# Kernel tuning notes

Hardware: AMD Instinct MI355X
Metric: run time of the kernel (lower is better)

The kernel has to match this reference:

```python
import jax, jax.numpy as jnp
import numpy as np
import math

B, SQ, SK, H, NH = 8, 512, 512, 768, 12
DH = H // NH

def setup_inputs() -> dict:
    key = jax.random.key(0)
    ks = jax.random.split(key, 8)
    s = 1.0 / math.sqrt(H)
    return {
        "hidden_states": jax.random.normal(ks[0], (B, SQ, H), jnp.float32),
        "context": jax.random.normal(ks[1], (B, SK, H), jnp.float32),
        "attention_mask": jax.random.randint(ks[2], (B, SK), 0, 2, jnp.int32),
        "Wq": jax.random.normal(ks[3], (H, H), jnp.float32) * s,
        "bq": jnp.zeros((H,), jnp.float32),
        "Wk": jax.random.normal(ks[4], (H, H), jnp.float32) * s,
        "bk": jnp.zeros((H,), jnp.float32),
        "Wv": jax.random.normal(ks[5], (H, H), jnp.float32) * s,
        "bv": jnp.zeros((H,), jnp.float32),
        "abs_pos_emb": jax.random.normal(ks[6], (512, DH), jnp.float32),
    }

def _heads(x):
    # [B, S, H] -> [B, NH, S, DH]
    b, s, _ = x.shape
    return x.reshape(b, s, NH, DH).transpose(0, 2, 1, 3)

def reference(hidden_states, context, attention_mask, Wq, bq, Wk, bk, Wv, bv, abs_pos_emb):
    q = _heads(hidden_states @ Wq.T + bq)   # [B,NH,SQ,DH]
    k = _heads(context @ Wk.T + bk)         # [B,NH,SK,DH]
    v = _heads(context @ Wv.T + bv)         # [B,NH,SK,DH]
    scores = jnp.einsum('bhqd,bhkd->bhqk', q, k)
    pos_k = abs_pos_emb[:context.shape[1]]          # [SK, DH]
    pos_q = abs_pos_emb[:hidden_states.shape[1]]    # [SQ, DH]
    pos_scores = jnp.einsum('bhqd,kd->bhqk', q + pos_q[None, None], pos_k)
    scores = (scores + pos_scores) / jnp.sqrt(jnp.float32(DH))
    mask_bias = jnp.where(attention_mask[:, None, None, :] == 0,
                          -jnp.inf, 0.0).astype(scores.dtype)
    scores = scores + mask_bias
    probs = jax.nn.softmax(scores, axis=-1)  # dropout is identity in eval
    out = jnp.einsum('bhqk,bhkd->bhqd', probs, v)
    b, _, sq, _ = out.shape
    return out.transpose(0, 2, 1, 3).reshape(b, sq, NH * DH)
```

## Files before the change

### kernel.cpp

```cpp
#include <hip/hip_runtime.h>
#include <stdint.h>

#define B_   8
#define SQ_  512
#define SK_  512
#define H_   768
#define NH_  12
#define DH_  64
#define BH_  (B_*NH_)
#define M_   (B_*SQ_)
#define NTOT (3*H_)

typedef __attribute__((ext_vector_type(8))) short short8;
typedef __attribute__((ext_vector_type(4))) float floatx4;
typedef __attribute__((ext_vector_type(4))) unsigned int uint4v;
typedef __attribute__((ext_vector_type(4))) unsigned short ushort4v;

#define MFMA16(a, b, c) __builtin_amdgcn_mfma_f32_16x16x32_bf16((a), (b), (c), 0, 0, 0)

__device__ __forceinline__ unsigned short f2b(float f) {
  union { float f; unsigned u; } c; c.f = f;
  unsigned r = (c.u + 0x7fffu + ((c.u >> 16) & 1u)) >> 16;
  return (unsigned short)r;
}
__device__ __forceinline__ float b2f(unsigned short u) {
  union { float f; unsigned u; } c; c.u = ((unsigned)u) << 16;
  return c.f;
}
__device__ __forceinline__ short8 ld8(const unsigned short* p) {
  union { uint4v u; short8 s; } c;
  c.u = *(const uint4v*)p;
  return c.s;
}

#define SEG_X   (M_*H_)
#define SEG_XC  (2*SEG_X)
#define SEG_W1  (H_*H_)
#define SEG_WE  (SEG_XC + 3*SEG_W1)
#define SEG_BE  (SEG_WE + NTOT)
#define SEG_PE  (SEG_BE + SQ_*DH_)

__global__ __launch_bounds__(256) void pack_kernel(
    const float* __restrict__ hid, const float* __restrict__ ctx,
    const float* __restrict__ Wq, const float* __restrict__ Wk, const float* __restrict__ Wv,
    const float* __restrict__ bq, const float* __restrict__ bk, const float* __restrict__ bv,
    const float* __restrict__ pos,
    unsigned short* __restrict__ Xh, unsigned short* __restrict__ Xc,
    unsigned short* __restrict__ Wa, float* __restrict__ Ba,
    unsigned short* __restrict__ Pb)
{
  int i = (blockIdx.x * 256 + threadIdx.x) * 4;
  if (i < SEG_X) {
    floatx4 v = *(const floatx4*)(hid + i);
    ushort4v o = { f2b(v.x), f2b(v.y), f2b(v.z), f2b(v.w) };
    *(ushort4v*)(Xh + i) = o;
  } else if (i < SEG_XC) {
    int j = i - SEG_X;
    floatx4 v = *(const floatx4*)(ctx + j);
    ushort4v o = { f2b(v.x), f2b(v.y), f2b(v.z), f2b(v.w) };
    *(ushort4v*)(Xc + j) = o;
  } else if (i < SEG_WE) {
    int j = i - SEG_XC;
    const float* src; int o;
    if (j < SEG_W1)        { src = Wq; o = j; }
    else if (j < 2*SEG_W1) { src = Wk; o = j - SEG_W1; }
    else                   { src = Wv; o = j - 2*SEG_W1; }
    floatx4 v = *(const floatx4*)(src + o);
    ushort4v ov = { f2b(v.x), f2b(v.y), f2b(v.z), f2b(v.w) };
    *(ushort4v*)(Wa + j) = ov;
  } else if (i < SEG_BE) {
    int j = i - SEG_WE;
    #pragma unroll
    for (int t = 0; t < 4; ++t) {
      int jj = j + t;
      float v = (jj < H_) ? bq[jj] : (jj < 2*H_) ? bk[jj - H_] : bv[jj - 2*H_];
      Ba[jj] = v;
    }
  } else if (i < SEG_PE) {
    int j = i - SEG_BE;
    floatx4 v = *(const floatx4*)(pos + j);
    ushort4v o = { f2b(v.x), f2b(v.y), f2b(v.z), f2b(v.w) };
    *(ushort4v*)(Pb + j) = o;
  }
}

__global__ __launch_bounds__(256) void qkv_gemm(
    const unsigned short* __restrict__ Xh, const unsigned short* __restrict__ Xc,
    const unsigned short* __restrict__ W,  const float* __restrict__ bias,
    const unsigned short* __restrict__ Pb,
    unsigned short* __restrict__ qw, unsigned short* __restrict__ kw,
    unsigned short* __restrict__ vt)
{
  __shared__ unsigned short As[128][72];
  __shared__ unsigned short Bs[128][72];

  int bx = blockIdx.x;
  int bn = bx % 18, bm = bx / 18;
  const unsigned short* X = (bn < 6) ? Xh : Xc;
  bool isV = (bn >= 12);
  int m0 = bm * 128, n0 = bn * 128;

  int tid = threadIdx.x;
  int lane = tid & 63, wave = tid >> 6;
  int wm = (wave & 1) * 64, wn = (wave >> 1) * 64;
  int lc16 = lane & 15, quad = lane >> 4, kk = quad * 8;
  int srow = tid >> 3, sch = (tid & 7) * 8;

  unsigned short (*TA)[72] = isV ? As : Bs;
  unsigned short (*TB)[72] = isV ? Bs : As;
  int oa = isV ? wm : wn;
  int ob = isV ? wn : wm;

  floatx4 acc[4][4];
  #pragma unroll
  for (int i = 0; i < 4; ++i)
    #pragma unroll
    for (int j = 0; j < 4; ++j) acc[i][j] = (floatx4){0.f, 0.f, 0.f, 0.f};

  for (int k0 = 0; k0 < H_; k0 += 64) {
    uint4v a[4], b[4];
    #pragma unroll
    for (int rp = 0; rp < 4; ++rp) {
      a[rp] = *(const uint4v*)&X[(m0 + srow + rp * 32) * H_ + k0 + sch];
      b[rp] = *(const uint4v*)&W[(n0 + srow + rp * 32) * H_ + k0 + sch];
    }
    __syncthreads();
    #pragma unroll
    for (int rp = 0; rp < 4; ++rp) {
      *(uint4v*)&As[srow + rp * 32][sch] = a[rp];
      *(uint4v*)&Bs[srow + rp * 32][sch] = b[rp];
    }
    __syncthreads();

    #pragma unroll
    for (int s = 0; s < 2; ++s) {
      short8 af[4], bf[4];
      #pragma unroll
      for (int i = 0; i < 4; ++i) af[i] = ld8(&TA[oa + i * 16 + lc16][s * 32 + kk]);
      #pragma unroll
      for (int i = 0; i < 4; ++i) bf[i] = ld8(&TB[ob + i * 16 + lc16][s * 32 + kk]);
      #pragma unroll
      for (int mi = 0; mi < 4; ++mi)
        #pragma unroll
        for (int ni = 0; ni < 4; ++ni)
          acc[mi][ni] = MFMA16(af[mi], bf[ni], acc[mi][ni]);
    }
  }

  if (!isV) {
    #pragma unroll
    for (int mi = 0; mi < 4; ++mi) {
      #pragma unroll
      for (int ni = 0; ni < 4; ++ni) {
        int gn0 = n0 + wn + mi * 16 + quad * 4;
        int gs  = m0 + wm + ni * 16 + lc16;
        int bidx = gs >> 9, s0 = gs & 511;
        floatx4 bv4 = *(const floatx4*)&bias[gn0];
        ushort4v o;
        if (gn0 < H_) {
          int h = gn0 >> 6, d0 = gn0 & 63;
          #pragma unroll
          for (int r = 0; r < 4; ++r) o[r] = f2b(acc[mi][ni][r] + bv4[r]);
          *(ushort4v*)(qw + (((bidx * NH_ + h) << 9) + s0) * DH_ + d0) = o;
        } else {
          int g = gn0 - H_;
          int h = g >> 6, d0 = g & 63;
          ushort4v pk = *(const ushort4v*)(Pb + s0 * DH_ + d0);
          #pragma unroll
          for (int r = 0; r < 4; ++r) o[r] = f2b(acc[mi][ni][r] + bv4[r] + b2f(pk[r]));
          *(ushort4v*)(kw + (((bidx * NH_ + h) << 9) + s0) * DH_ + d0) = o;
        }
      }
    }
  } else {
    #pragma unroll
    for (int mi = 0; mi < 4; ++mi) {
      #pragma unroll
      for (int ni = 0; ni < 4; ++ni) {
        int gm0 = m0 + wm + mi * 16 + quad * 4;
        int gn  = n0 + wn + ni * 16 + lc16;
        float bv = bias[gn];
        int bidx = gm0 >> 9, s0 = gm0 & 511;
        int g = gn - 2 * H_;
        int h = g >> 6, d = g & 63;
        ushort4v pk;
        #pragma unroll
        for (int r = 0; r < 4; ++r) pk[r] = f2b(acc[mi][ni][r] + bv);
        *(ushort4v*)(vt + ((bidx * NH_ + h) * DH_ + d) * SK_ + s0) = pk;
      }
    }
  }
}

#define SCALE2 0.18033688011112042f
#define CPAD 136

__global__ __launch_bounds__(256) void attn_kernel(
    const unsigned short* __restrict__ qw, const unsigned short* __restrict__ kw,
    const unsigned short* __restrict__ vt, const unsigned short* __restrict__ posb,
    const int* __restrict__ mask, float* __restrict__ out)
{
  __shared__ unsigned short Sc[64][CPAD];
  __shared__ float mb2[SK_];
  __shared__ float red[64][4];

  int bx = blockIdx.x;
  int bh = bx >> 3, qt = bx & 7;
  int b = bh / NH_, h = bh - b * NH_;
  int tid = threadIdx.x, lane = tid & 63, wave = tid >> 6;
  int lc16 = lane & 15, quad = lane >> 4, kk = quad * 8;

  for (int i = tid; i < SK_; i += 256)
    mb2[i] = mask[(b << 9) + i] ? 0.0f : -100000.0f;

  const unsigned short* qbase = qw + ((bh << 9) + qt * 64) * DH_;
  const unsigned short* pqb   = posb + (qt * 64) * DH_;
  short8 aq[4][2], ap[4][2];
  #pragma unroll
  for (int rt = 0; rt < 4; ++rt) {
    const unsigned short* qr = qbase + (rt * 16 + lc16) * DH_;
    const unsigned short* pr = pqb + (rt * 16 + lc16) * DH_;
    aq[rt][0] = ld8(qr + kk);
    aq[rt][1] = ld8(qr + 32 + kk);
    ap[rt][0] = ld8(pr + kk);
    ap[rt][1] = ld8(pr + 32 + kk);
  }

  const unsigned short* vb0 = vt + (bh * DH_ + wave * 16 + lc16) * SK_;
  float rs[4] = {0.f, 0.f, 0.f, 0.f};
  floatx4 o[4];
  #pragma unroll
  for (int i = 0; i < 4; ++i) o[i] = (floatx4){0.f, 0.f, 0.f, 0.f};

  __syncthreads();

  for (int chunk = 0; chunk < 4; ++chunk) {
    #pragma unroll
    for (int ct = 0; ct < 2; ++ct) {
      int kcol = chunk * 128 + wave * 32 + ct * 16;
      const unsigned short* kb = kw + ((bh << 9) + kcol) * DH_;
      const unsigned short* pb = posb + kcol * DH_;
      short8 b0 = ld8(kb + lc16 * DH_ + kk);
      short8 b1 = ld8(kb + lc16 * DH_ + 32 + kk);
      short8 p0 = ld8(pb + lc16 * DH_ + kk);
      short8 p1 = ld8(pb + lc16 * DH_ + 32 + kk);
      floatx4 mk = *(const floatx4*)&mb2[kcol + quad * 4];
      floatx4 c[4];
      #pragma unroll
      for (int rt = 0; rt < 4; ++rt) {
        c[rt] = (floatx4){0.f, 0.f, 0.f, 0.f};
        c[rt] = MFMA16(b0, aq[rt][0], c[rt]);
        c[rt] = MFMA16(b1, aq[rt][1], c[rt]);
        c[rt] = MFMA16(p0, ap[rt][0], c[rt]);
        c[rt] = MFMA16(p1, ap[rt][1], c[rt]);
      }
      int lcol = wave * 32 + ct * 16 + quad * 4;
      #pragma unroll
      for (int rt = 0; rt < 4; ++rt) {
        ushort4v pv;
        float s = 0.f;
        #pragma unroll
        for (int r = 0; r < 4; ++r) {
          float e = __builtin_exp2f(c[rt][r] * SCALE2 + mk[r]);
          s += e;
          pv[r] = f2b(e);
        }
        rs[rt] += s;
        *(ushort4v*)&Sc[rt * 16 + lc16][lcol] = pv;
      }
    }
    __syncthreads();

    #pragma unroll
    for (int ks = 0; ks < 4; ++ks) {
      short8 vf = ld8(vb0 + chunk * 128 + ks * 32 + kk);
      #pragma unroll
      for (int rt = 0; rt < 4; ++rt) {
        short8 pa = ld8(&Sc[rt * 16 + lc16][ks * 32 + kk]);
        o[rt] = MFMA16(pa, vf, o[rt]);
      }
    }
    __syncthreads();
  }

  #pragma unroll
  for (int rt = 0; rt < 4; ++rt) {
    rs[rt] += __shfl_xor(rs[rt], 16, 64);
    rs[rt] += __shfl_xor(rs[rt], 32, 64);
  }
  if (quad == 0) {
    #pragma unroll
    for (int rt = 0; rt < 4; ++rt) red[rt * 16 + lc16][wave] = rs[rt];
  }
  __syncthreads();

  #pragma unroll
  for (int rt = 0; rt < 4; ++rt) {
    #pragma unroll
    for (int r = 0; r < 4; ++r) {
      int sl = rt * 16 + quad * 4 + r;
      float inv = 1.0f / (red[sl][0] + red[sl][1] + red[sl][2] + red[sl][3]);
      int s = qt * 64 + sl;
      out[((b << 9) + s) * H_ + h * DH_ + wave * 16 + lc16] = o[rt][r] * inv;
    }
  }
}

extern "C" void kernel_launch(void* const* d_in, const int* in_sizes, int n_in,
                              void* d_out, int out_size, void* d_ws, size_t ws_size,
                              hipStream_t stream) {
  (void)in_sizes; (void)n_in; (void)out_size; (void)ws_size;
  const float* hid  = (const float*)d_in[0];
  const float* ctx  = (const float*)d_in[1];
  const int*   mask = (const int*)d_in[2];
  const float* Wq   = (const float*)d_in[3];
  const float* bq   = (const float*)d_in[4];
  const float* Wk   = (const float*)d_in[5];
  const float* bk   = (const float*)d_in[6];
  const float* Wv   = (const float*)d_in[7];
  const float* bv   = (const float*)d_in[8];
  const float* pos  = (const float*)d_in[9];

  char* ws = (char*)d_ws;
  size_t off = 0;
  auto alloc = [&](size_t bytes) { char* p = ws + off; off = (off + bytes + 255) & ~(size_t)255; return p; };
  unsigned short* Xh = (unsigned short*)alloc((size_t)SEG_X * 2);
  unsigned short* Xc = (unsigned short*)alloc((size_t)SEG_X * 2);
  unsigned short* Wa = (unsigned short*)alloc((size_t)3 * SEG_W1 * 2);
  float*          Ba = (float*)alloc((size_t)NTOT * 4);
  unsigned short* qw = (unsigned short*)alloc((size_t)BH_ * SQ_ * DH_ * 2);
  unsigned short* kw = (unsigned short*)alloc((size_t)BH_ * SK_ * DH_ * 2);
  unsigned short* vt = (unsigned short*)alloc((size_t)BH_ * DH_ * SK_ * 2);
  unsigned short* Pb = (unsigned short*)alloc((size_t)SQ_ * DH_ * 2);

  int pack_blocks = (SEG_PE / 4 + 255) / 256;
  pack_kernel<<<pack_blocks, 256, 0, stream>>>(hid, ctx, Wq, Wk, Wv, bq, bk, bv, pos, Xh, Xc, Wa, Ba, Pb);
  qkv_gemm<<<32 * 18, 256, 0, stream>>>(Xh, Xc, Wa, Ba, Pb, qw, kw, vt);
  attn_kernel<<<BH_ * 8, 256, 0, stream>>>(qw, kw, vt, Pb, mask, (float*)d_out);
}
```

Measured before the change: 173.8 us.

## Prefetch global tiles in QKV GEMM and double-buffer attention score staging

The QKV GEMM now loads the next K-slice of X and W into registers while computing on the current LDS tile, and its block index is remapped so blocks sharing the same A/B tiles land on the same XCD. The attention kernel software-prefetches the next K/pos fragments and V fragments ahead of use. It double-buffers the score tile in LDS, which drops the trailing barrier per chunk, and reorders the grid so blocks with the same batch-head are spread across the grid. This hides global load latency and barrier stalls at the cost of more registers and twice the score LDS.

```diff
diff --git a/kernel.cpp b/kernel.cpp
--- a/kernel.cpp
+++ b/kernel.cpp
@@ -95,7 +95,9 @@
   __shared__ unsigned short Bs[128][72];
 
   int bx = blockIdx.x;
-  int bn = bx % 18, bm = bx / 18;
+  int xcd = bx & 7, j = bx >> 3;
+  int bm = (xcd >> 1) * 8 + j / 9;
+  int bn = (xcd & 1) * 9 + j % 9;
   const unsigned short* X = (bn < 6) ? Xh : Xc;
   bool isV = (bn >= 12);
   int m0 = bm * 128, n0 = bn * 128;
@@ -115,15 +117,16 @@
   #pragma unroll
   for (int i = 0; i < 4; ++i)
     #pragma unroll
-    for (int j = 0; j < 4; ++j) acc[i][j] = (floatx4){0.f, 0.f, 0.f, 0.f};
+    for (int jj = 0; jj < 4; ++jj) acc[i][jj] = (floatx4){0.f, 0.f, 0.f, 0.f};
+
+  uint4v a[4], b[4];
+  #pragma unroll
+  for (int rp = 0; rp < 4; ++rp) {
+    a[rp] = *(const uint4v*)&X[(m0 + srow + rp * 32) * H_ + sch];
+    b[rp] = *(const uint4v*)&W[(n0 + srow + rp * 32) * H_ + sch];
+  }
 
   for (int k0 = 0; k0 < H_; k0 += 64) {
-    uint4v a[4], b[4];
-    #pragma unroll
-    for (int rp = 0; rp < 4; ++rp) {
-      a[rp] = *(const uint4v*)&X[(m0 + srow + rp * 32) * H_ + k0 + sch];
-      b[rp] = *(const uint4v*)&W[(n0 + srow + rp * 32) * H_ + k0 + sch];
-    }
     __syncthreads();
     #pragma unroll
     for (int rp = 0; rp < 4; ++rp) {
@@ -131,6 +134,14 @@
       *(uint4v*)&Bs[srow + rp * 32][sch] = b[rp];
     }
     __syncthreads();
+
+    if (k0 + 64 < H_) {
+      #pragma unroll
+      for (int rp = 0; rp < 4; ++rp) {
+        a[rp] = *(const uint4v*)&X[(m0 + srow + rp * 32) * H_ + k0 + 64 + sch];
+        b[rp] = *(const uint4v*)&W[(n0 + srow + rp * 32) * H_ + k0 + 64 + sch];
+      }
+    }
 
     #pragma unroll
     for (int s = 0; s < 2; ++s) {
@@ -200,12 +211,12 @@
     const unsigned short* __restrict__ vt, const unsigned short* __restrict__ posb,
     const int* __restrict__ mask, float* __restrict__ out)
 {
-  __shared__ unsigned short Sc[64][CPAD];
+  __shared__ unsigned short Sc[2][64][CPAD];
   __shared__ float mb2[SK_];
   __shared__ float red[64][4];
 
   int bx = blockIdx.x;
-  int bh = bx >> 3, qt = bx & 7;
+  int bh = bx % 96, qt = bx / 96;
   int b = bh / NH_, h = bh - b * NH_;
   int tid = threadIdx.x, lane = tid & 63, wave = tid >> 6;
   int lc16 = lane & 15, quad = lane >> 4, kk = quad * 8;
@@ -226,61 +237,82 @@
     ap[rt][1] = ld8(pr + 32 + kk);
   }
 
+  const unsigned short* kwb = kw + ((bh << 9)) * DH_;
   const unsigned short* vb0 = vt + (bh * DH_ + wave * 16 + lc16) * SK_;
   float rs[4] = {0.f, 0.f, 0.f, 0.f};
   floatx4 o[4];
   #pragma unroll
   for (int i = 0; i < 4; ++i) o[i] = (floatx4){0.f, 0.f, 0.f, 0.f};
 
+  short8 cb0, cb1, cp0, cp1, nb0, nb1, np0, np1;
+  {
+    int kcol = wave * 32;
+    const unsigned short* kb = kwb + kcol * DH_;
+    const unsigned short* pb = posb + kcol * DH_;
+    cb0 = ld8(kb + lc16 * DH_ + kk);
+    cb1 = ld8(kb + lc16 * DH_ + 32 + kk);
+    cp0 = ld8(pb + lc16 * DH_ + kk);
+    cp1 = ld8(pb + lc16 * DH_ + 32 + kk);
+  }
+
   __syncthreads();
 
   for (int chunk = 0; chunk < 4; ++chunk) {
+    unsigned short (*S)[CPAD] = Sc[chunk & 1];
+
+    short8 vf[4];
+    #pragma unroll
+    for (int ks = 0; ks < 4; ++ks) vf[ks] = ld8(vb0 + chunk * 128 + ks * 32 + kk);
+
     #pragma unroll
     for (int ct = 0; ct < 2; ++ct) {
+      int s = chunk * 2 + ct;
+      if (s < 7) {
+        int kcol = ((s + 1) >> 1) * 128 + wave * 32 + ((s + 1) & 1) * 16;
+        const unsigned short* kb = kwb + kcol * DH_;
+        const unsigned short* pb = posb + kcol * DH_;
+        nb0 = ld8(kb + lc16 * DH_ + kk);
+        nb1 = ld8(kb + lc16 * DH_ + 32 + kk);
+        np0 = ld8(pb + lc16 * DH_ + kk);
+        np1 = ld8(pb + lc16 * DH_ + 32 + kk);
+      }
       int kcol = chunk * 128 + wave * 32 + ct * 16;
-      const unsigned short* kb = kw + ((bh << 9) + kcol) * DH_;
-      const unsigned short* pb = posb + kcol * DH_;
-      short8 b0 = ld8(kb + lc16 * DH_ + kk);
-      short8 b1 = ld8(kb + lc16 * DH_ + 32 + kk);
-      short8 p0 = ld8(pb + lc16 * DH_ + kk);
-      short8 p1 = ld8(pb + lc16 * DH_ + 32 + kk);
       floatx4 mk = *(const floatx4*)&mb2[kcol + quad * 4];
       floatx4 c[4];
       #pragma unroll
       for (int rt = 0; rt < 4; ++rt) {
         c[rt] = (floatx4){0.f, 0.f, 0.f, 0.f};
-        c[rt] = MFMA16(b0, aq[rt][0], c[rt]);
-        c[rt] = MFMA16(b1, aq[rt][1], c[rt]);
-        c[rt] = MFMA16(p0, ap[rt][0], c[rt]);
-        c[rt] = MFMA16(p1, ap[rt][1], c[rt]);
+        c[rt] = MFMA16(cb0, aq[rt][0], c[rt]);
+        c[rt] = MFMA16(cb1, aq[rt][1], c[rt]);
+        c[rt] = MFMA16(cp0, ap[rt][0], c[rt]);
+        c[rt] = MFMA16(cp1, ap[rt][1], c[rt]);
       }
       int lcol = wave * 32 + ct * 16 + quad * 4;
       #pragma unroll
       for (int rt = 0; rt < 4; ++rt) {
         ushort4v pv;
-        float s = 0.f;
+        float sum = 0.f;
         #pragma unroll
         for (int r = 0; r < 4; ++r) {
           float e = __builtin_exp2f(c[rt][r] * SCALE2 + mk[r]);
-          s += e;
+          sum += e;
           pv[r] = f2b(e);
         }
-        rs[rt] += s;
-        *(ushort4v*)&Sc[rt * 16 + lc16][lcol] = pv;
-      }
+        rs[rt] += sum;
+        *(ushort4v*)&S[rt * 16 + lc16][lcol] = pv;
+      }
+      cb0 = nb0; cb1 = nb1; cp0 = np0; cp1 = np1;
     }
     __syncthreads();
 
     #pragma unroll
     for (int ks = 0; ks < 4; ++ks) {
-      short8 vf = ld8(vb0 + chunk * 128 + ks * 32 + kk);
       #pragma unroll
       for (int rt = 0; rt < 4; ++rt) {
-        short8 pa = ld8(&Sc[rt * 16 + lc16][ks * 32 + kk]);
-        o[rt] = MFMA16(pa, vf, o[rt]);
-      }
-    }
-    __syncthreads();
+        short8 pa = ld8(&S[rt * 16 + lc16][ks * 32 + kk]);
+        o[rt] = MFMA16(pa, vf[ks], o[rt]);
+      }
+    }
   }
 
   #pragma unroll
```

Measured after the change: 155.4 us. 10.6% less time.
